# Optimization experiments

Hardware: AMD Instinct MI355X
Metric: run time of the kernel (lower is better)

Reference implementation:

```python
import jax, jax.numpy as jnp
import numpy as np

N_NODES = 100000
N_EDGES = 1600000
IN_DIM = 128
OUT_DIM = 128
NEG_SLOPE = 0.2


def setup_inputs() -> dict:
    key = jax.random.key(0)
    ks = jax.random.split(key, 7)
    x = jax.random.normal(ks[0], (N_NODES, IN_DIM), dtype=jnp.float32)
    edge_index = jax.random.randint(ks[1], (2, N_EDGES), 0, N_NODES, dtype=jnp.int32)
    # xavier-ish scale for [in, out] weight layout (y = x @ W)
    s = float(np.sqrt(2.0 / (IN_DIM + OUT_DIM)))
    W_q = jax.random.normal(ks[2], (IN_DIM, OUT_DIM), dtype=jnp.float32) * s
    W_k = jax.random.normal(ks[3], (IN_DIM, OUT_DIM), dtype=jnp.float32) * s
    W_v = jax.random.normal(ks[4], (IN_DIM, OUT_DIM), dtype=jnp.float32) * s
    W_l = jax.random.normal(ks[5], (IN_DIM, OUT_DIM), dtype=jnp.float32) * s
    b_l = jnp.zeros((OUT_DIM,), dtype=jnp.float32)
    return {"x": x, "edge_index": edge_index, "W_q": W_q, "W_k": W_k,
            "W_v": W_v, "W_l": W_l, "b_l": b_l}


def reference(x, edge_index, W_q, W_k, W_v, W_l, b_l):
    num_nodes = x.shape[0]
    row, col = edge_index[0], edge_index[1]

    h_q = x @ W_q                                   # [N, D]
    h_k = x @ W_k                                   # [N, D]
    _h_v = x @ W_v                                  # computed in original, unused downstream

    # aggregated query: sum of neighbor queries per destination node
    q_agg = jax.ops.segment_sum(h_q[col], row, num_segments=num_nodes)  # [N, D]
    k_act = jax.nn.leaky_relu(h_k, NEG_SLOPE)

    # per-edge attention scores (note: original uses raw q_agg, not activated)
    scores = jnp.sum(k_act[row] * q_agg[col], axis=1) / (OUT_DIM ** 0.5)  # [E]

    # scatter-softmax over edges grouped by destination (row)
    max_val = jax.ops.segment_max(scores, row, num_segments=num_nodes)
    exp_scores = jnp.exp(scores - max_val[row])
    sum_exp = jax.ops.segment_sum(exp_scores, row, num_segments=num_nodes)
    alpha = exp_scores / (sum_exp[row] + 1e-8)      # [E]; dropout is identity in eval

    h_proj = x @ W_l + b_l                          # [N, D]
    weighted = alpha[:, None] * h_proj[col]         # [E, D]
    h_prime = jax.ops.segment_sum(weighted, row, num_segments=num_nodes)
    return jax.nn.leaky_relu(h_prime, NEG_SLOPE)
```

## Files before the change

kernel.cpp:

```cpp
#include <hip/hip_runtime.h>
#include <math.h>

#define N_NODES 100000
#define N_EDGES 1600000
#define DIM 128
#define CAP 64

#define NB1 196
#define NPB 512
#define CHUNK1 4096
#define GRID1 391
#define SLOT1 52
#define LSTRIDE 197

typedef short bf16x8 __attribute__((ext_vector_type(8)));
typedef float f32x4 __attribute__((ext_vector_type(4)));

static __device__ __forceinline__ unsigned bf16rne(float f) {
    unsigned u = __float_as_uint(f);
    return (u + 0x7FFFu + ((u >> 16) & 1u)) >> 16;
}
static __device__ __forceinline__ float bflo(unsigned u) { return __uint_as_float(u << 16); }
static __device__ __forceinline__ float bfhi(unsigned u) { return __uint_as_float(u & 0xFFFF0000u); }


__global__ __launch_bounds__(256) void pb_k(
    const float* __restrict__ x, const float* __restrict__ Wq,
    const float* __restrict__ Wk, const float* __restrict__ Wl,
    const int* __restrict__ row, const int* __restrict__ col,
    ushort* __restrict__ xb, ushort* __restrict__ kactb,
    ushort* __restrict__ WqTh, ushort* __restrict__ WqTl,
    ushort* __restrict__ WlTh, ushort* __restrict__ WlTl,
    unsigned* __restrict__ bkt, int* __restrict__ bktc) {
    __shared__ uint4 smem4[2625];
    int j = blockIdx.x, t = threadIdx.x;

    if (j % 3 == 2) {
        int blk = j / 3;
        int* lcnt = (int*)smem4;
        unsigned* lbuf = (unsigned*)smem4 + 256;
        if (t < NB1) lcnt[t] = 0;
        __syncthreads();
        long base = (long)blk * CHUNK1;
        if (base + CHUNK1 <= N_EDGES) {
            const uint4* r4 = (const uint4*)row + (size_t)blk * 1024;
            const uint4* c4 = (const uint4*)col + (size_t)blk * 1024;
#pragma unroll
            for (int q = 0; q < 4; q++) {
                uint4 rv = r4[q * 256 + t];
                uint4 cv = c4[q * 256 + t];
                unsigned rr[4] = {rv.x, rv.y, rv.z, rv.w};
                unsigned cc[4] = {cv.x, cv.y, cv.z, cv.w};
#pragma unroll
                for (int i = 0; i < 4; i++) {
                    int b = rr[i] >> 9;
                    int p = atomicAdd(&lcnt[b], 1);
                    if (p < SLOT1) lbuf[p * LSTRIDE + b] = (cc[i] << 9) | (rr[i] & 511u);
                }
            }
        } else {
            for (int i = t; base + i < N_EDGES; i += 256) {
                unsigned r = (unsigned)row[base + i], c = (unsigned)col[base + i];
                int b = r >> 9;
                int p = atomicAdd(&lcnt[b], 1);
                if (p < SLOT1) lbuf[p * LSTRIDE + b] = (c << 9) | (r & 511u);
            }
        }
        __syncthreads();
        if (t < NB1) bktc[(size_t)blk * NB1 + t] = min(lcnt[t], SLOT1);
        int wave = t >> 6, lane = t & 63;
        for (int s = wave; s < NB1; s += 4) {
            if (lane < min(lcnt[s], SLOT1))
                bkt[((size_t)s * GRID1 + blk) * SLOT1 + lane] = lbuf[lane * LSTRIDE + s];
        }
        return;
    }

    int p = (j / 3) * 2 + (j % 3);
    ushort* bw = (ushort*)smem4;

    if (p < 2) {
        const float* W = (p == 0) ? Wq : Wl;
        ushort* Th = (p == 0) ? WqTh : WlTh;
        ushort* Tl = (p == 0) ? WqTl : WlTl;
        for (int i = t; i < 16384; i += 256) {
            int k = i >> 7, n = i & 127;
            float v = W[i];
            unsigned hi = bf16rne(v);
            float lo = v - bflo(hi);
            Th[n * 128 + k] = (ushort)hi;
            Tl[n * 128 + k] = (ushort)bf16rne(lo);
        }
    }
    for (int i = t; i < 16384; i += 256) {
        int k = i >> 7, n = i & 127;
        bw[n * 136 + k] = (ushort)bf16rne(Wk[i]);
    }

    int wave = t >> 6, lane = t & 63;
    int ln15 = lane & 15, quad = lane >> 4;
    long base = (long)p * 128 + wave * 32;

    bf16x8 Af[2][4];
#pragma unroll
    for (int r = 0; r < 2; r++) {
        long rw = base + r * 16 + ln15;
        long rowc = rw < N_NODES ? rw : N_NODES - 1;
#pragma unroll
        for (int s = 0; s < 4; s++) {
            int ch = s * 4 + quad;
            const float4* xp = (const float4*)(x + rowc * 128 + ch * 8);
            float4 u0 = xp[0], u1 = xp[1];
            bf16x8 f;
            f[0] = (short)bf16rne(u0.x); f[1] = (short)bf16rne(u0.y);
            f[2] = (short)bf16rne(u0.z); f[3] = (short)bf16rne(u0.w);
            f[4] = (short)bf16rne(u1.x); f[5] = (short)bf16rne(u1.y);
            f[6] = (short)bf16rne(u1.z); f[7] = (short)bf16rne(u1.w);
            Af[r][s] = f;
            if (rw < N_NODES) *(bf16x8*)(xb + rw * 128 + ch * 8) = f;
        }
    }
    f32x4 acc[2][8];
#pragma unroll
    for (int r = 0; r < 2; r++)
#pragma unroll
        for (int t8 = 0; t8 < 8; t8++) acc[r][t8] = (f32x4){0.f, 0.f, 0.f, 0.f};

    __syncthreads();
#pragma unroll
    for (int s = 0; s < 4; s++) {
#pragma unroll
        for (int t8 = 0; t8 < 8; t8++) {
            bf16x8 b = *(const bf16x8*)(bw + (t8 * 16 + ln15) * 136 + (s * 4 + quad) * 8);
            acc[0][t8] = __builtin_amdgcn_mfma_f32_16x16x32_bf16(Af[0][s], b, acc[0][t8], 0, 0, 0);
            acc[1][t8] = __builtin_amdgcn_mfma_f32_16x16x32_bf16(Af[1][s], b, acc[1][t8], 0, 0, 0);
        }
    }
    __syncthreads();
    for (int i = t; i < 16384; i += 256) {
        int k = i >> 7, n = i & 127;
        float v = Wk[i];
        unsigned hi = bf16rne(v);
        float lo = v - bflo(hi);
        bw[n * 136 + k] = (ushort)bf16rne(lo);
    }
    __syncthreads();
#pragma unroll
    for (int s = 0; s < 4; s++) {
#pragma unroll
        for (int t8 = 0; t8 < 8; t8++) {
            bf16x8 b = *(const bf16x8*)(bw + (t8 * 16 + ln15) * 136 + (s * 4 + quad) * 8);
            acc[0][t8] = __builtin_amdgcn_mfma_f32_16x16x32_bf16(Af[0][s], b, acc[0][t8], 0, 0, 0);
            acc[1][t8] = __builtin_amdgcn_mfma_f32_16x16x32_bf16(Af[1][s], b, acc[1][t8], 0, 0, 0);
        }
    }
#pragma unroll
    for (int r = 0; r < 2; r++) {
#pragma unroll
        for (int reg = 0; reg < 4; reg++) {
            long node = base + r * 16 + quad * 4 + reg;
            if (node < N_NODES) {
#pragma unroll
                for (int t8 = 0; t8 < 8; t8++) {
                    float v = acc[r][t8][reg];
                    v = v > 0.f ? v : 0.2f * v;
                    kactb[node * 128 + t8 * 16 + ln15] = (ushort)bf16rne(v);
                }
            }
        }
    }
}


__global__ __launch_bounds__(1024) void build_k(const int* __restrict__ bktc,
                                                const unsigned* __restrict__ bkt,
                                                int* __restrict__ cur,
                                                int* __restrict__ scol) {
    __shared__ int lcur[NPB];
    __shared__ int lc[GRID1];
    int b = blockIdx.x, t = threadIdx.x;
    if (t < NPB) lcur[t] = 0;
    if (t < GRID1) lc[t] = bktc[(size_t)t * NB1 + b];
    __syncthreads();
    int wave = t >> 6, lane = t & 63;
    const unsigned* D = bkt + (size_t)b * GRID1 * SLOT1;
    for (int s = wave; s < GRID1; s += 16) {
        if (lane < lc[s]) {
            unsigned v = D[(size_t)s * SLOT1 + lane];
            int rl = (int)(v & 511u);
            int c = (int)(v >> 9);
            int p = atomicAdd(&lcur[rl], 1);
            if (p < CAP) scol[((size_t)b * NPB + rl) * CAP + p] = c;
        }
    }
    __syncthreads();
    if (t < NPB) {
        int node = b * NPB + t;
        if (node < N_NODES) cur[node] = lcur[t];
    }
}


__global__ __launch_bounds__(256) void xq_k(const uint4* __restrict__ xb4,
                                            const int* __restrict__ cur,
                                            const int* __restrict__ scol,
                                            const ushort* __restrict__ BTh,
                                            const ushort* __restrict__ BTl,
                                            uint4* __restrict__ qx4) {
    __shared__ ushort lxa[16][136];
    __shared__ ushort lq[16][136];
    int t = threadIdx.x;
    int wave = t >> 6, lane = t & 63;
    int e = lane >> 4;
    int gl = lane & 15;
    long blkbase = (long)blockIdx.x * 16;

#pragma unroll
    for (int i = 0; i < 4; i++) {
        int li = wave * 4 + i;
        long node = blkbase + li;
        int d = min(cur[node], CAP);
        int cb = (lane < d) ? scol[node * CAP + lane] : 0;
        float a0 = 0.f, a1 = 0.f, a2 = 0.f, a3 = 0.f;
        float a4 = 0.f, a5 = 0.f, a6 = 0.f, a7 = 0.f;
        int k = 0;
        for (; k + 8 <= d; k += 8) {
            int c0 = __shfl(cb, k + e, 64);
            int c1 = __shfl(cb, k + 4 + e, 64);
            uint4 u0 = xb4[(size_t)c0 * 16 + gl];
            uint4 u1 = xb4[(size_t)c1 * 16 + gl];
            a0 += bflo(u0.x); a1 += bfhi(u0.x); a2 += bflo(u0.y); a3 += bfhi(u0.y);
            a4 += bflo(u0.z); a5 += bfhi(u0.z); a6 += bflo(u0.w); a7 += bfhi(u0.w);
            a0 += bflo(u1.x); a1 += bfhi(u1.x); a2 += bflo(u1.y); a3 += bfhi(u1.y);
            a4 += bflo(u1.z); a5 += bfhi(u1.z); a6 += bflo(u1.w); a7 += bfhi(u1.w);
        }
        for (; k < d; k += 4) {
            int c = __shfl(cb, k + e, 64);
            uint4 u = xb4[(size_t)c * 16 + gl];
            if (k + e < d) {
                a0 += bflo(u.x); a1 += bfhi(u.x); a2 += bflo(u.y); a3 += bfhi(u.y);
                a4 += bflo(u.z); a5 += bfhi(u.z); a6 += bflo(u.w); a7 += bfhi(u.w);
            }
        }
        a0 += __shfl_xor(a0, 16, 64); a1 += __shfl_xor(a1, 16, 64);
        a2 += __shfl_xor(a2, 16, 64); a3 += __shfl_xor(a3, 16, 64);
        a4 += __shfl_xor(a4, 16, 64); a5 += __shfl_xor(a5, 16, 64);
        a6 += __shfl_xor(a6, 16, 64); a7 += __shfl_xor(a7, 16, 64);
        a0 += __shfl_xor(a0, 32, 64); a1 += __shfl_xor(a1, 32, 64);
        a2 += __shfl_xor(a2, 32, 64); a3 += __shfl_xor(a3, 32, 64);
        a4 += __shfl_xor(a4, 32, 64); a5 += __shfl_xor(a5, 32, 64);
        a6 += __shfl_xor(a6, 32, 64); a7 += __shfl_xor(a7, 32, 64);
        if (e == 0) {
            uint4 o;
            o.x = bf16rne(a0) | (bf16rne(a1) << 16);
            o.y = bf16rne(a2) | (bf16rne(a3) << 16);
            o.z = bf16rne(a4) | (bf16rne(a5) << 16);
            o.w = bf16rne(a6) | (bf16rne(a7) << 16);
            *(uint4*)&lxa[li][gl * 8] = o;
        }
    }
    __syncthreads();

    int ln15 = lane & 15, quad = (lane >> 4) & 3;
    const bf16x8* Bh8 = (const bf16x8*)BTh;
    const bf16x8* Bl8 = (const bf16x8*)BTl;
    bf16x8 af[4];
#pragma unroll
    for (int s = 0; s < 4; s++)
        af[s] = *(const bf16x8*)&lxa[ln15][(s * 4 + quad) * 8];
#pragma unroll
    for (int ti = 0; ti < 2; ti++) {
        int ct = wave * 2 + ti;
        f32x4 acc = (f32x4){0.f, 0.f, 0.f, 0.f};
#pragma unroll
        for (int phase = 0; phase < 2; phase++) {
            const bf16x8* B8 = phase ? Bl8 : Bh8;
#pragma unroll
            for (int s = 0; s < 4; s++)
                acc = __builtin_amdgcn_mfma_f32_16x16x32_bf16(
                    af[s], B8[(ct * 16 + ln15) * 16 + s * 4 + quad], acc, 0, 0, 0);
        }
#pragma unroll
        for (int reg = 0; reg < 4; reg++)
            lq[quad * 4 + reg][ct * 16 + ln15] = (ushort)bf16rne(acc[reg]);
    }
    __syncthreads();

    const uint2* xb2 = (const uint2*)xb4;
#pragma unroll
    for (int i = 0; i < 2; i++) {
        int idx = i * 256 + t;
        int g = idx >> 5, c = idx & 31;
        long n2 = blkbase + g;
        uint2 q2 = *(const uint2*)&lq[g][c * 4];
        uint2 x2 = xb2[n2 * 32 + c];
        qx4[n2 * 32 + c] = make_uint4(q2.x, q2.y, x2.x, x2.y);
    }
}


__global__ __launch_bounds__(256) void attn_k(const uint2* __restrict__ kactb,
                                              const uint4* __restrict__ qx4,
                                              const int* __restrict__ cur,
                                              const int* __restrict__ scol,
                                              uint2* __restrict__ xwb,
                                              float* __restrict__ sumw) {
    long g = (blockIdx.x * 256 + threadIdx.x) >> 6;
    int lane = threadIdx.x & 63;
    int l31 = lane & 31;
    int h = lane >> 5;
    int d = min(cur[g], CAP);
    uint2 ku = kactb[(size_t)g * 32 + l31];
    const float scale = 0.08838834764831845f;
    float k0 = bflo(ku.x) * scale, k1 = bfhi(ku.x) * scale;
    float k2 = bflo(ku.y) * scale, k3 = bfhi(ku.y) * scale;

    int cb = (lane < d) ? scol[g * CAP + lane] : 0;
    float S = 0.f;
    float a0 = 0.f, a1 = 0.f, a2 = 0.f, a3 = 0.f;
    int k = 0;
    for (; k + 8 <= d; k += 8) {
        int c0 = __shfl(cb, k + h, 64);
        int c1 = __shfl(cb, k + 2 + h, 64);
        int c2 = __shfl(cb, k + 4 + h, 64);
        int c3 = __shfl(cb, k + 6 + h, 64);
        uint4 u0 = qx4[(size_t)c0 * 32 + l31];
        uint4 u1 = qx4[(size_t)c1 * 32 + l31];
        uint4 u2 = qx4[(size_t)c2 * 32 + l31];
        uint4 u3 = qx4[(size_t)c3 * 32 + l31];
        float p0 = k0 * bflo(u0.x) + k1 * bfhi(u0.x) + k2 * bflo(u0.y) + k3 * bfhi(u0.y);
        float p1 = k0 * bflo(u1.x) + k1 * bfhi(u1.x) + k2 * bflo(u1.y) + k3 * bfhi(u1.y);
        float p2 = k0 * bflo(u2.x) + k1 * bfhi(u2.x) + k2 * bflo(u2.y) + k3 * bfhi(u2.y);
        float p3 = k0 * bflo(u3.x) + k1 * bfhi(u3.x) + k2 * bflo(u3.y) + k3 * bfhi(u3.y);
#pragma unroll
        for (int off = 16; off > 0; off >>= 1) {
            p0 += __shfl_xor(p0, off, 32); p1 += __shfl_xor(p1, off, 32);
            p2 += __shfl_xor(p2, off, 32); p3 += __shfl_xor(p3, off, 32);
        }
        float e0 = __expf(p0), e1 = __expf(p1);
        float e2 = __expf(p2), e3 = __expf(p3);
        S += (e0 + e1) + (e2 + e3);
        a0 += e0 * bflo(u0.z) + e1 * bflo(u1.z) + e2 * bflo(u2.z) + e3 * bflo(u3.z);
        a1 += e0 * bfhi(u0.z) + e1 * bfhi(u1.z) + e2 * bfhi(u2.z) + e3 * bfhi(u3.z);
        a2 += e0 * bflo(u0.w) + e1 * bflo(u1.w) + e2 * bflo(u2.w) + e3 * bflo(u3.w);
        a3 += e0 * bfhi(u0.w) + e1 * bfhi(u1.w) + e2 * bfhi(u2.w) + e3 * bfhi(u3.w);
    }
    for (; k + 2 <= d; k += 2) {
        int c = __shfl(cb, k + h, 64);
        uint4 u = qx4[(size_t)c * 32 + l31];
        float p = k0 * bflo(u.x) + k1 * bfhi(u.x) + k2 * bflo(u.y) + k3 * bfhi(u.y);
#pragma unroll
        for (int off = 16; off > 0; off >>= 1) p += __shfl_xor(p, off, 32);
        float e0 = __expf(p);
        S += e0;
        a0 += e0 * bflo(u.z);
        a1 += e0 * bfhi(u.z);
        a2 += e0 * bflo(u.w);
        a3 += e0 * bfhi(u.w);
    }
    if (k < d) {
        int c = __shfl(cb, k, 64);
        uint4 u = qx4[(size_t)c * 32 + l31];
        float p = k0 * bflo(u.x) + k1 * bfhi(u.x) + k2 * bflo(u.y) + k3 * bfhi(u.y);
#pragma unroll
        for (int off = 16; off > 0; off >>= 1) p += __shfl_xor(p, off, 32);
        float e0 = __expf(p);
        if (h == 0) {
            S += e0;
            a0 += e0 * bflo(u.z);
            a1 += e0 * bfhi(u.z);
            a2 += e0 * bflo(u.w);
            a3 += e0 * bfhi(u.w);
        }
    }
    S += __shfl_xor(S, 32, 64);
    a0 += __shfl_xor(a0, 32, 64);
    a1 += __shfl_xor(a1, 32, 64);
    a2 += __shfl_xor(a2, 32, 64);
    a3 += __shfl_xor(a3, 32, 64);
    float inv = 1.f / (S + 1e-8f);
    if (h == 0) {
        uint2 o;
        o.x = bf16rne(a0 * inv) | (bf16rne(a1 * inv) << 16);
        o.y = bf16rne(a2 * inv) | (bf16rne(a3 * inv) << 16);
        xwb[(size_t)g * 32 + l31] = o;
        if (l31 == 0) sumw[g] = S * inv;
    }
}


__global__ __launch_bounds__(256) void fin_k(const ushort* __restrict__ Ab,
                                             const ushort* __restrict__ BTh,
                                             const ushort* __restrict__ BTl,
                                             const float* __restrict__ bl,
                                             const float* __restrict__ sumw,
                                             float* __restrict__ out) {
    int tid = threadIdx.x;
    int wave = tid >> 6, lane = tid & 63;
    int ln15 = lane & 15, quad = (lane >> 4) & 3;
    long base = (long)blockIdx.x * 128 + wave * 32;

    const bf16x8* A8 = (const bf16x8*)Ab;
    const bf16x8* Bh8 = (const bf16x8*)BTh;
    const bf16x8* Bl8 = (const bf16x8*)BTl;

    bf16x8 Af[2][4];
#pragma unroll
    for (int r = 0; r < 2; r++) {
        long row = base + r * 16 + ln15;
#pragma unroll
        for (int s = 0; s < 4; s++) Af[r][s] = A8[row * 16 + s * 4 + quad];
    }
    float blv[8];
#pragma unroll
    for (int t = 0; t < 8; t++) blv[t] = bl[t * 16 + ln15];

    f32x4 acc[2][8];
#pragma unroll
    for (int r = 0; r < 2; r++)
#pragma unroll
        for (int t = 0; t < 8; t++) acc[r][t] = (f32x4){0.f, 0.f, 0.f, 0.f};

#pragma unroll
    for (int phase = 0; phase < 2; phase++) {
        const bf16x8* B8 = phase ? Bl8 : Bh8;
#pragma unroll
        for (int s = 0; s < 4; s++) {
#pragma unroll
            for (int t = 0; t < 8; t++) {
                bf16x8 b = B8[(t * 16 + ln15) * 16 + s * 4 + quad];
                acc[0][t] = __builtin_amdgcn_mfma_f32_16x16x32_bf16(Af[0][s], b, acc[0][t], 0, 0, 0);
                acc[1][t] = __builtin_amdgcn_mfma_f32_16x16x32_bf16(Af[1][s], b, acc[1][t], 0, 0, 0);
            }
        }
    }
#pragma unroll
    for (int r = 0; r < 2; r++) {
#pragma unroll
        for (int reg = 0; reg < 4; reg++) {
            long node = base + r * 16 + quad * 4 + reg;
            if (node < N_NODES) {
                float sw = sumw[node];
#pragma unroll
                for (int t = 0; t < 8; t++) {
                    float v = acc[r][t][reg] + sw * blv[t];
                    v = v > 0.f ? v : 0.2f * v;
                    out[node * 128 + t * 16 + ln15] = v;
                }
            }
        }
    }
}


extern "C" void kernel_launch(void* const* d_in, const int* in_sizes, int n_in,
                              void* d_out, int out_size, void* d_ws, size_t ws_size,
                              hipStream_t stream) {
    const float* x  = (const float*)d_in[0];
    const int* row  = (const int*)d_in[1];
    const int* col  = row + N_EDGES;
    const float* Wq = (const float*)d_in[2];
    const float* Wk = (const float*)d_in[3];
    const float* Wl = (const float*)d_in[5];
    const float* bl = (const float*)d_in[6];
    float* out = (float*)d_out;

    ushort* xb    = (ushort*)d_ws;
    ushort* qx    = xb + (size_t)N_NODES * DIM;
    ushort* kactb = qx + (size_t)N_NODES * 256;
    ushort* xwb   = kactb + (size_t)N_NODES * DIM;
    ushort* wbuf  = xwb + (size_t)N_NODES * DIM;
    ushort* WqTh = wbuf,             *WqTl = wbuf + 16384;
    ushort* WlTh = wbuf + 2 * 16384, *WlTl = wbuf + 3 * 16384;
    float* sumw = (float*)(wbuf + 4 * 16384);
    int* cur  = (int*)(sumw + N_NODES);
    int* scol = cur + N_NODES;
    unsigned* bkt = (unsigned*)(scol + (size_t)N_NODES * CAP);
    int* bktc = (int*)(bkt + (size_t)NB1 * GRID1 * SLOT1);

    pb_k<<<1173, 256, 0, stream>>>(x, Wq, Wk, Wl, row, col, xb, kactb,
                                   WqTh, WqTl, WlTh, WlTl, bkt, bktc);
    build_k<<<NB1, 1024, 0, stream>>>(bktc, bkt, cur, scol);
    xq_k<<<N_NODES / 16, 256, 0, stream>>>((const uint4*)xb, cur, scol,
                                           WqTh, WqTl, (uint4*)qx);
    attn_k<<<N_NODES / 4, 256, 0, stream>>>((const uint2*)kactb, (const uint4*)qx,
                                            cur, scol, (uint2*)xwb, sumw);
    fin_k<<<(N_NODES + 127) / 128, 256, 0, stream>>>(xwb, WlTh, WlTl, bl, sumw, out);
}
```

Before: 462.3 us.

## Reassociate score product: fold Wq into key side, gather raw x aggregates

Rather than projecting aggregated neighbor features through Wq per node, the score k_act·(A x Wq) is rewritten as (k_act Wq^T)·(A x). The first kernel now computes kq = k_act·Wq^T via a second split-bf16 MFMA pass, staging k_act in LDS. The aggregation kernel becomes a pure neighbor-sum of bf16 x with no matmul, using one 16-lane group per node. This removes the MFMA and LDS staging from the aggregation stage but adds GEMM work, LDS use and an extra bf16 rounding of k_act before the Wq product in the first kernel.

```diff
diff --git a/kernel.cpp b/kernel.cpp
--- a/kernel.cpp
+++ b/kernel.cpp
@@ -28,11 +28,10 @@
     const float* __restrict__ x, const float* __restrict__ Wq,
     const float* __restrict__ Wk, const float* __restrict__ Wl,
     const int* __restrict__ row, const int* __restrict__ col,
-    ushort* __restrict__ xb, ushort* __restrict__ kactb,
-    ushort* __restrict__ WqTh, ushort* __restrict__ WqTl,
+    ushort* __restrict__ xb, ushort* __restrict__ kq,
     ushort* __restrict__ WlTh, ushort* __restrict__ WlTl,
     unsigned* __restrict__ bkt, int* __restrict__ bktc) {
-    __shared__ uint4 smem4[2625];
+    __shared__ uint4 smem4[4352];
     int j = blockIdx.x, t = threadIdx.x;
 
     if (j % 3 == 2) {
@@ -77,24 +76,21 @@
     }
 
     int p = (j / 3) * 2 + (j % 3);
-    ushort* bw = (ushort*)smem4;
-
-    if (p < 2) {
-        const float* W = (p == 0) ? Wq : Wl;
-        ushort* Th = (p == 0) ? WqTh : WlTh;
-        ushort* Tl = (p == 0) ? WqTl : WlTl;
+    ushort* b1 = (ushort*)smem4;
+    ushort* b2 = b1 + 17408;
+
+    if (p == 0) {
         for (int i = t; i < 16384; i += 256) {
             int k = i >> 7, n = i & 127;
-            float v = W[i];
+            float v = Wl[i];
             unsigned hi = bf16rne(v);
-            float lo = v - bflo(hi);
-            Th[n * 128 + k] = (ushort)hi;
-            Tl[n * 128 + k] = (ushort)bf16rne(lo);
+            WlTh[n * 128 + k] = (ushort)hi;
+            WlTl[n * 128 + k] = (ushort)bf16rne(v - bflo(hi));
         }
     }
     for (int i = t; i < 16384; i += 256) {
         int k = i >> 7, n = i & 127;
-        bw[n * 136 + k] = (ushort)bf16rne(Wk[i]);
+        b2[n * 136 + k] = (ushort)bf16rne(Wk[i]);
     }
 
     int wave = t >> 6, lane = t & 63;
@@ -131,7 +127,7 @@
     for (int s = 0; s < 4; s++) {
 #pragma unroll
         for (int t8 = 0; t8 < 8; t8++) {
-            bf16x8 b = *(const bf16x8*)(bw + (t8 * 16 + ln15) * 136 + (s * 4 + quad) * 8);
+            bf16x8 b = *(const bf16x8*)(b2 + (t8 * 16 + ln15) * 136 + (s * 4 + quad) * 8);
             acc[0][t8] = __builtin_amdgcn_mfma_f32_16x16x32_bf16(Af[0][s], b, acc[0][t8], 0, 0, 0);
             acc[1][t8] = __builtin_amdgcn_mfma_f32_16x16x32_bf16(Af[1][s], b, acc[1][t8], 0, 0, 0);
         }
@@ -141,17 +137,75 @@
         int k = i >> 7, n = i & 127;
         float v = Wk[i];
         unsigned hi = bf16rne(v);
-        float lo = v - bflo(hi);
-        bw[n * 136 + k] = (ushort)bf16rne(lo);
+        b2[n * 136 + k] = (ushort)bf16rne(v - bflo(hi));
     }
     __syncthreads();
 #pragma unroll
     for (int s = 0; s < 4; s++) {
 #pragma unroll
         for (int t8 = 0; t8 < 8; t8++) {
-            bf16x8 b = *(const bf16x8*)(bw + (t8 * 16 + ln15) * 136 + (s * 4 + quad) * 8);
+            bf16x8 b = *(const bf16x8*)(b2 + (t8 * 16 + ln15) * 136 + (s * 4 + quad) * 8);
             acc[0][t8] = __builtin_amdgcn_mfma_f32_16x16x32_bf16(Af[0][s], b, acc[0][t8], 0, 0, 0);
             acc[1][t8] = __builtin_amdgcn_mfma_f32_16x16x32_bf16(Af[1][s], b, acc[1][t8], 0, 0, 0);
+        }
+    }
+#pragma unroll
+    for (int r = 0; r < 2; r++) {
+#pragma unroll
+        for (int reg = 0; reg < 4; reg++) {
+            int rl = wave * 32 + r * 16 + quad * 4 + reg;
+#pragma unroll
+            for (int t8 = 0; t8 < 8; t8++) {
+                float v = acc[r][t8][reg];
+                v = v > 0.f ? v : 0.2f * v;
+                b1[rl * 136 + t8 * 16 + ln15] = (ushort)bf16rne(v);
+            }
+        }
+    }
+    __syncthreads();
+    for (int i = t; i < 16384; i += 256) {
+        b2[(i >> 7) * 136 + (i & 127)] = (ushort)bf16rne(Wq[i]);
+    }
+    __syncthreads();
+#pragma unroll
+    for (int r = 0; r < 2; r++)
+#pragma unroll
+        for (int t8 = 0; t8 < 8; t8++) acc[r][t8] = (f32x4){0.f, 0.f, 0.f, 0.f};
+#pragma unroll
+    for (int r = 0; r < 2; r++) {
+        bf16x8 af[4];
+#pragma unroll
+        for (int s = 0; s < 4; s++)
+            af[s] = *(const bf16x8*)(b1 + (wave * 32 + r * 16 + ln15) * 136 + (s * 4 + quad) * 8);
+#pragma unroll
+        for (int s = 0; s < 4; s++) {
+#pragma unroll
+            for (int t8 = 0; t8 < 8; t8++) {
+                bf16x8 b = *(const bf16x8*)(b2 + (t8 * 16 + ln15) * 136 + (s * 4 + quad) * 8);
+                acc[r][t8] = __builtin_amdgcn_mfma_f32_16x16x32_bf16(af[s], b, acc[r][t8], 0, 0, 0);
+            }
+        }
+    }
+    __syncthreads();
+    for (int i = t; i < 16384; i += 256) {
+        float v = Wq[i];
+        unsigned hi = bf16rne(v);
+        b2[(i >> 7) * 136 + (i & 127)] = (ushort)bf16rne(v - bflo(hi));
+    }
+    __syncthreads();
+#pragma unroll
+    for (int r = 0; r < 2; r++) {
+        bf16x8 af[4];
+#pragma unroll
+        for (int s = 0; s < 4; s++)
+            af[s] = *(const bf16x8*)(b1 + (wave * 32 + r * 16 + ln15) * 136 + (s * 4 + quad) * 8);
+#pragma unroll
+        for (int s = 0; s < 4; s++) {
+#pragma unroll
+            for (int t8 = 0; t8 < 8; t8++) {
+                bf16x8 b = *(const bf16x8*)(b2 + (t8 * 16 + ln15) * 136 + (s * 4 + quad) * 8);
+                acc[r][t8] = __builtin_amdgcn_mfma_f32_16x16x32_bf16(af[s], b, acc[r][t8], 0, 0, 0);
+            }
         }
     }
 #pragma unroll
@@ -161,11 +215,8 @@
             long node = base + r * 16 + quad * 4 + reg;
             if (node < N_NODES) {
 #pragma unroll
-                for (int t8 = 0; t8 < 8; t8++) {
-                    float v = acc[r][t8][reg];
-                    v = v > 0.f ? v : 0.2f * v;
-                    kactb[node * 128 + t8 * 16 + ln15] = (ushort)bf16rne(v);
-                }
+                for (int t8 = 0; t8 < 8; t8++)
+                    kq[node * 128 + t8 * 16 + ln15] = (ushort)bf16rne(acc[r][t8][reg]);
             }
         }
     }
@@ -201,106 +252,57 @@
 }
 
 
-__global__ __launch_bounds__(256) void xq_k(const uint4* __restrict__ xb4,
+__global__ __launch_bounds__(256) void xa_k(const uint4* __restrict__ xb4,
                                             const int* __restrict__ cur,
                                             const int* __restrict__ scol,
-                                            const ushort* __restrict__ BTh,
-                                            const ushort* __restrict__ BTl,
-                                            uint4* __restrict__ qx4) {
-    __shared__ ushort lxa[16][136];
-    __shared__ ushort lq[16][136];
-    int t = threadIdx.x;
-    int wave = t >> 6, lane = t & 63;
-    int e = lane >> 4;
-    int gl = lane & 15;
-    long blkbase = (long)blockIdx.x * 16;
-
-#pragma unroll
-    for (int i = 0; i < 4; i++) {
-        int li = wave * 4 + i;
-        long node = blkbase + li;
-        int d = min(cur[node], CAP);
-        int cb = (lane < d) ? scol[node * CAP + lane] : 0;
-        float a0 = 0.f, a1 = 0.f, a2 = 0.f, a3 = 0.f;
-        float a4 = 0.f, a5 = 0.f, a6 = 0.f, a7 = 0.f;
+                                            uint4* __restrict__ ax4) {
+    int g = (blockIdx.x * 256 + threadIdx.x) >> 4;
+    int gl = threadIdx.x & 15;
+    int d = min(cur[g], CAP);
+    float a0 = 0.f, a1 = 0.f, a2 = 0.f, a3 = 0.f;
+    float a4 = 0.f, a5 = 0.f, a6 = 0.f, a7 = 0.f;
+    for (int j = 0; j < d; j += 16) {
+        int cb = (j + gl < d) ? scol[(size_t)g * CAP + j + gl] : 0;
+        int lim = min(16, d - j);
         int k = 0;
-        for (; k + 8 <= d; k += 8) {
-            int c0 = __shfl(cb, k + e, 64);
-            int c1 = __shfl(cb, k + 4 + e, 64);
+        for (; k + 4 <= lim; k += 4) {
+            int c0 = __shfl(cb, k, 16),     c1 = __shfl(cb, k + 1, 16);
+            int c2 = __shfl(cb, k + 2, 16), c3 = __shfl(cb, k + 3, 16);
             uint4 u0 = xb4[(size_t)c0 * 16 + gl];
             uint4 u1 = xb4[(size_t)c1 * 16 + gl];
+            uint4 u2 = xb4[(size_t)c2 * 16 + gl];
+            uint4 u3 = xb4[(size_t)c3 * 16 + gl];
             a0 += bflo(u0.x); a1 += bfhi(u0.x); a2 += bflo(u0.y); a3 += bfhi(u0.y);
             a4 += bflo(u0.z); a5 += bfhi(u0.z); a6 += bflo(u0.w); a7 += bfhi(u0.w);
             a0 += bflo(u1.x); a1 += bfhi(u1.x); a2 += bflo(u1.y); a3 += bfhi(u1.y);
             a4 += bflo(u1.z); a5 += bfhi(u1.z); a6 += bflo(u1.w); a7 += bfhi(u1.w);
-        }
-        for (; k < d; k += 4) {
-            int c = __shfl(cb, k + e, 64);
+            a0 += bflo(u2.x); a1 += bfhi(u2.x); a2 += bflo(u2.y); a3 += bfhi(u2.y);
+            a4 += bflo(u2.z); a5 += bfhi(u2.z); a6 += bflo(u2.w); a7 += bfhi(u2.w);
+            a0 += bflo(u3.x); a1 += bfhi(u3.x); a2 += bflo(u3.y); a3 += bfhi(u3.y);
+            a4 += bflo(u3.z); a5 += bfhi(u3.z); a6 += bflo(u3.w); a7 += bfhi(u3.w);
+        }
+        for (; k < lim; k++) {
+            int c = __shfl(cb, k, 16);
             uint4 u = xb4[(size_t)c * 16 + gl];
-            if (k + e < d) {
-                a0 += bflo(u.x); a1 += bfhi(u.x); a2 += bflo(u.y); a3 += bfhi(u.y);
-                a4 += bflo(u.z); a5 += bfhi(u.z); a6 += bflo(u.w); a7 += bfhi(u.w);
-            }
-        }
-        a0 += __shfl_xor(a0, 16, 64); a1 += __shfl_xor(a1, 16, 64);
-        a2 += __shfl_xor(a2, 16, 64); a3 += __shfl_xor(a3, 16, 64);
-        a4 += __shfl_xor(a4, 16, 64); a5 += __shfl_xor(a5, 16, 64);
-        a6 += __shfl_xor(a6, 16, 64); a7 += __shfl_xor(a7, 16, 64);
-        a0 += __shfl_xor(a0, 32, 64); a1 += __shfl_xor(a1, 32, 64);
-        a2 += __shfl_xor(a2, 32, 64); a3 += __shfl_xor(a3, 32, 64);
-        a4 += __shfl_xor(a4, 32, 64); a5 += __shfl_xor(a5, 32, 64);
-        a6 += __shfl_xor(a6, 32, 64); a7 += __shfl_xor(a7, 32, 64);
-        if (e == 0) {
-            uint4 o;
-            o.x = bf16rne(a0) | (bf16rne(a1) << 16);
-            o.y = bf16rne(a2) | (bf16rne(a3) << 16);
-            o.z = bf16rne(a4) | (bf16rne(a5) << 16);
-            o.w = bf16rne(a6) | (bf16rne(a7) << 16);
-            *(uint4*)&lxa[li][gl * 8] = o;
-        }
-    }
-    __syncthreads();
-
-    int ln15 = lane & 15, quad = (lane >> 4) & 3;
-    const bf16x8* Bh8 = (const bf16x8*)BTh;
-    const bf16x8* Bl8 = (const bf16x8*)BTl;
-    bf16x8 af[4];
-#pragma unroll
-    for (int s = 0; s < 4; s++)
-        af[s] = *(const bf16x8*)&lxa[ln15][(s * 4 + quad) * 8];
-#pragma unroll
-    for (int ti = 0; ti < 2; ti++) {
-        int ct = wave * 2 + ti;
-        f32x4 acc = (f32x4){0.f, 0.f, 0.f, 0.f};
-#pragma unroll
-        for (int phase = 0; phase < 2; phase++) {
-            const bf16x8* B8 = phase ? Bl8 : Bh8;
-#pragma unroll
-            for (int s = 0; s < 4; s++)
-                acc = __builtin_amdgcn_mfma_f32_16x16x32_bf16(
-                    af[s], B8[(ct * 16 + ln15) * 16 + s * 4 + quad], acc, 0, 0, 0);
-        }
-#pragma unroll
-        for (int reg = 0; reg < 4; reg++)
-            lq[quad * 4 + reg][ct * 16 + ln15] = (ushort)bf16rne(acc[reg]);
-    }
-    __syncthreads();
-
+            a0 += bflo(u.x); a1 += bfhi(u.x); a2 += bflo(u.y); a3 += bfhi(u.y);
+            a4 += bflo(u.z); a5 += bfhi(u.z); a6 += bflo(u.w); a7 += bfhi(u.w);
+        }
+    }
+    uint4 o;
+    o.x = bf16rne(a0) | (bf16rne(a1) << 16);
+    o.y = bf16rne(a2) | (bf16rne(a3) << 16);
+    o.z = bf16rne(a4) | (bf16rne(a5) << 16);
+    o.w = bf16rne(a6) | (bf16rne(a7) << 16);
     const uint2* xb2 = (const uint2*)xb4;
-#pragma unroll
-    for (int i = 0; i < 2; i++) {
-        int idx = i * 256 + t;
-        int g = idx >> 5, c = idx & 31;
-        long n2 = blkbase + g;
-        uint2 q2 = *(const uint2*)&lq[g][c * 4];
-        uint2 x2 = xb2[n2 * 32 + c];
-        qx4[n2 * 32 + c] = make_uint4(q2.x, q2.y, x2.x, x2.y);
-    }
-}
-
-
-__global__ __launch_bounds__(256) void attn_k(const uint2* __restrict__ kactb,
-                                              const uint4* __restrict__ qx4,
+    uint2 xp0 = xb2[(size_t)g * 32 + 2 * gl];
+    uint2 xp1 = xb2[(size_t)g * 32 + 2 * gl + 1];
+    ax4[(size_t)g * 32 + 2 * gl]     = make_uint4(o.x, o.y, xp0.x, xp0.y);
+    ax4[(size_t)g * 32 + 2 * gl + 1] = make_uint4(o.z, o.w, xp1.x, xp1.y);
+}
+
+
+__global__ __launch_bounds__(256) void attn_k(const uint2* __restrict__ kq2,
+                                              const uint4* __restrict__ ax4,
                                               const int* __restrict__ cur,
                                               const int* __restrict__ scol,
                                               uint2* __restrict__ xwb,
@@ -310,12 +312,12 @@
     int l31 = lane & 31;
     int h = lane >> 5;
     int d = min(cur[g], CAP);
-    uint2 ku = kactb[(size_t)g * 32 + l31];
+    uint2 ku = kq2[(size_t)g * 32 + l31];
     const float scale = 0.08838834764831845f;
     float k0 = bflo(ku.x) * scale, k1 = bfhi(ku.x) * scale;
     float k2 = bflo(ku.y) * scale, k3 = bfhi(ku.y) * scale;
 
-    int cb = (lane < d) ? scol[g * CAP + lane] : 0;
+    int cb = (lane < d) ? scol[(size_t)g * CAP + lane] : 0;
     float S = 0.f;
     float a0 = 0.f, a1 = 0.f, a2 = 0.f, a3 = 0.f;
     int k = 0;
@@ -324,10 +326,10 @@
         int c1 = __shfl(cb, k + 2 + h, 64);
         int c2 = __shfl(cb, k + 4 + h, 64);
         int c3 = __shfl(cb, k + 6 + h, 64);
-        uint4 u0 = qx4[(size_t)c0 * 32 + l31];
-        uint4 u1 = qx4[(size_t)c1 * 32 + l31];
-        uint4 u2 = qx4[(size_t)c2 * 32 + l31];
-        uint4 u3 = qx4[(size_t)c3 * 32 + l31];
+        uint4 u0 = ax4[(size_t)c0 * 32 + l31];
+        uint4 u1 = ax4[(size_t)c1 * 32 + l31];
+        uint4 u2 = ax4[(size_t)c2 * 32 + l31];
+        uint4 u3 = ax4[(size_t)c3 * 32 + l31];
         float p0 = k0 * bflo(u0.x) + k1 * bfhi(u0.x) + k2 * bflo(u0.y) + k3 * bfhi(u0.y);
         float p1 = k0 * bflo(u1.x) + k1 * bfhi(u1.x) + k2 * bflo(u1.y) + k3 * bfhi(u1.y);
         float p2 = k0 * bflo(u2.x) + k1 * bfhi(u2.x) + k2 * bflo(u2.y) + k3 * bfhi(u2.y);
@@ -347,7 +349,7 @@
     }
     for (; k + 2 <= d; k += 2) {
         int c = __shfl(cb, k + h, 64);
-        uint4 u = qx4[(size_t)c * 32 + l31];
+        uint4 u = ax4[(size_t)c * 32 + l31];
         float p = k0 * bflo(u.x) + k1 * bfhi(u.x) + k2 * bflo(u.y) + k3 * bfhi(u.y);
 #pragma unroll
         for (int off = 16; off > 0; off >>= 1) p += __shfl_xor(p, off, 32);
@@ -360,7 +362,7 @@
     }
     if (k < d) {
         int c = __shfl(cb, k, 64);
-        uint4 u = qx4[(size_t)c * 32 + l31];
+        uint4 u = ax4[(size_t)c * 32 + l31];
         float p = k0 * bflo(u.x) + k1 * bfhi(u.x) + k2 * bflo(u.y) + k3 * bfhi(u.y);
 #pragma unroll
         for (int off = 16; off > 0; off >>= 1) p += __shfl_xor(p, off, 32);
@@ -466,24 +468,22 @@
     float* out = (float*)d_out;
 
     ushort* xb    = (ushort*)d_ws;
-    ushort* qx    = xb + (size_t)N_NODES * DIM;
-    ushort* kactb = qx + (size_t)N_NODES * 256;
-    ushort* xwb   = kactb + (size_t)N_NODES * DIM;
+    ushort* ax    = xb + (size_t)N_NODES * DIM;
+    ushort* kq    = ax + (size_t)N_NODES * 256;
+    ushort* xwb   = kq + (size_t)N_NODES * DIM;
     ushort* wbuf  = xwb + (size_t)N_NODES * DIM;
-    ushort* WqTh = wbuf,             *WqTl = wbuf + 16384;
-    ushort* WlTh = wbuf + 2 * 16384, *WlTl = wbuf + 3 * 16384;
-    float* sumw = (float*)(wbuf + 4 * 16384);
+    ushort* WlTh = wbuf, *WlTl = wbuf + 16384;
+    float* sumw = (float*)(wbuf + 2 * 16384);
     int* cur  = (int*)(sumw + N_NODES);
     int* scol = cur + N_NODES;
     unsigned* bkt = (unsigned*)(scol + (size_t)N_NODES * CAP);
     int* bktc = (int*)(bkt + (size_t)NB1 * GRID1 * SLOT1);
 
-    pb_k<<<1173, 256, 0, stream>>>(x, Wq, Wk, Wl, row, col, xb, kactb,
-                                   WqTh, WqTl, WlTh, WlTl, bkt, bktc);
+    pb_k<<<1173, 256, 0, stream>>>(x, Wq, Wk, Wl, row, col, xb, kq,
+                                   WlTh, WlTl, bkt, bktc);
     build_k<<<NB1, 1024, 0, stream>>>(bktc, bkt, cur, scol);
-    xq_k<<<N_NODES / 16, 256, 0, stream>>>((const uint4*)xb, cur, scol,
-                                           WqTh, WqTl, (uint4*)qx);
-    attn_k<<<N_NODES / 4, 256, 0, stream>>>((const uint2*)kactb, (const uint4*)qx,
+    xa_k<<<N_NODES / 16, 256, 0, stream>>>((const uint4*)xb, cur, scol, (uint4*)ax);
+    attn_k<<<N_NODES / 4, 256, 0, stream>>>((const uint2*)kq, (const uint4*)ax,
                                             cur, scol, (uint2*)xwb, sumw);
     fin_k<<<(N_NODES + 127) / 128, 256, 0, stream>>>(xwb, WlTh, WlTl, bl, sumw, out);
 }
```

Result: faster. 450.2 us (-2.6%).
